# Optimization experiments

Measured on AMD Instinct MI355X. Metric: run time of the kernel, lower is better.

## Reference

```python
import jax, jax.numpy as jnp
import numpy as np

NEG_SLOPE = 0.2


def setup_inputs() -> dict:
    key = jax.random.key(0)
    k1, k2, k3 = jax.random.split(key, 3)
    bs, n_agents, input_dim = 32, 512, 128
    n_heads, hidden_dim = 8, 64
    h = jax.random.normal(k1, (bs, n_agents, input_dim), dtype=jnp.float32)
    # Linear(input_dim, n_heads*hidden_dim, bias=False), stored as [in, out]
    W = jax.random.normal(k2, (input_dim, n_heads * hidden_dim), dtype=jnp.float32) * (1.0 / np.sqrt(input_dim))
    # xavier_uniform with gain=1.414 on shape (1, n_heads, 2*hidden_dim)
    fan = n_heads + 2 * hidden_dim
    bound = 1.414 * np.sqrt(6.0 / fan)
    att_a = jax.random.uniform(k3, (1, n_heads, 2 * hidden_dim), dtype=jnp.float32,
                               minval=-bound, maxval=bound)
    return {"h": h, "W": W, "att_a": att_a}


def reference(h, W, att_a):
    bs, n_agents, _ = h.shape
    n_heads = att_a.shape[1]
    hidden_dim = att_a.shape[2] // 2
    # h_prime: [bs, n_heads, n_agents, hidden_dim]
    h_prime = (h @ W).reshape(bs, n_agents, n_heads, hidden_dim).transpose(0, 2, 1, 3)
    # Additive score decomposes exactly: (a1.h_i + a2.h_j) == sum(cat(h_i,h_j)*a)
    a_src = att_a[0, :, :hidden_dim]   # [n_heads, hidden_dim]
    a_dst = att_a[0, :, hidden_dim:]   # [n_heads, hidden_dim]
    e_src = jnp.einsum('bhnd,hd->bhn', h_prime, a_src)  # score contribution of node i (row)
    e_dst = jnp.einsum('bhnd,hd->bhn', h_prime, a_dst)  # contribution of node j (col)
    e = e_src[:, :, :, None] + e_dst[:, :, None, :]     # [bs, n_heads, n, n]
    e = jnp.where(e >= 0, e, NEG_SLOPE * e)             # leaky_relu(0.2)
    attention = jax.nn.softmax(e, axis=-1)
    h_new = jnp.einsum('bhnm,bhmd->bhnd', attention, h_prime)
    return jax.nn.elu(h_new)
```

## Files before the change

### kernel.cpp

```cpp
#include <hip/hip_runtime.h>

#define BS 32
#define NA 512
#define ID 128
#define NH 8
#define HD 64
#define NHD 512
#define NEG 0.2f
#define NC 32
#define CH 16

__global__ __launch_bounds__(256) void k1_gemm(
    const float* __restrict__ h, const float* __restrict__ W,
    const float* __restrict__ att, float* __restrict__ hp,
    float* __restrict__ s_out, float* __restrict__ t_out) {
  int blk = blockIdx.x;
  int b = blk >> 5;
  int n0 = (blk & 31) * 16;
  int t = threadIdx.x;
  int lane = t & 63, w = t >> 6;
  int r0 = __builtin_amdgcn_readfirstlane((w >> 1) * 8);
  int chalf = __builtin_amdgcn_readfirstlane(w & 1);
  int col = chalf * 256 + lane * 4;
  int head = col >> 6;
  int d0 = col & 63;
  const float* arow = h + ((size_t)b * NA + n0 + r0) * ID;
  const float* wptr = W + col;

  float4 a0c = {0,0,0,0}, a1c = {0,0,0,0}, a2c = {0,0,0,0}, a3c = {0,0,0,0};
  float4 a4c = {0,0,0,0}, a5c = {0,0,0,0}, a6c = {0,0,0,0}, a7c = {0,0,0,0};

#define K1_ROW(I, C, KK)                                                      \
  { float a_ = arow[(I) * ID + kc + (KK)];                                    \
    C.x += a_ * wv.x; C.y += a_ * wv.y; C.z += a_ * wv.z; C.w += a_ * wv.w; }
  #pragma unroll 1
  for (int kc = 0; kc < ID; kc += 8) {
    #pragma unroll
    for (int kk = 0; kk < 8; ++kk) {
      float4 wv = *(const float4*)(wptr + (size_t)(kc + kk) * NHD);
      K1_ROW(0, a0c, kk) K1_ROW(1, a1c, kk) K1_ROW(2, a2c, kk)
      K1_ROW(3, a3c, kk) K1_ROW(4, a4c, kk) K1_ROW(5, a5c, kk)
      K1_ROW(6, a6c, kk) K1_ROW(7, a7c, kk)
    }
  }
#undef K1_ROW
  {
    size_t off = ((((size_t)b * NH + head) * NA) + (n0 + r0)) * HD + d0;
    *(float4*)(hp + off) = a0c; off += HD;
    *(float4*)(hp + off) = a1c; off += HD;
    *(float4*)(hp + off) = a2c; off += HD;
    *(float4*)(hp + off) = a3c; off += HD;
    *(float4*)(hp + off) = a4c; off += HD;
    *(float4*)(hp + off) = a5c; off += HD;
    *(float4*)(hp + off) = a6c; off += HD;
    *(float4*)(hp + off) = a7c;
  }
  {
    float4 as4 = *(const float4*)(att + head * 128 + d0);
    float4 ad4 = *(const float4*)(att + head * 128 + 64 + d0);
#define DOT4(C, A) ((C).x*(A).x + (C).y*(A).y + (C).z*(A).z + (C).w*(A).w)
    float sp0 = DOT4(a0c, as4), tp0 = DOT4(a0c, ad4);
    float sp1 = DOT4(a1c, as4), tp1 = DOT4(a1c, ad4);
    float sp2 = DOT4(a2c, as4), tp2 = DOT4(a2c, ad4);
    float sp3 = DOT4(a3c, as4), tp3 = DOT4(a3c, ad4);
    float sp4 = DOT4(a4c, as4), tp4 = DOT4(a4c, ad4);
    float sp5 = DOT4(a5c, as4), tp5 = DOT4(a5c, ad4);
    float sp6 = DOT4(a6c, as4), tp6 = DOT4(a6c, ad4);
    float sp7 = DOT4(a7c, as4), tp7 = DOT4(a7c, ad4);
#undef DOT4
    #pragma unroll
    for (int m = 1; m < 16; m <<= 1) {
      sp0 += __shfl_xor(sp0, m, 64); tp0 += __shfl_xor(tp0, m, 64);
      sp1 += __shfl_xor(sp1, m, 64); tp1 += __shfl_xor(tp1, m, 64);
      sp2 += __shfl_xor(sp2, m, 64); tp2 += __shfl_xor(tp2, m, 64);
      sp3 += __shfl_xor(sp3, m, 64); tp3 += __shfl_xor(tp3, m, 64);
      sp4 += __shfl_xor(sp4, m, 64); tp4 += __shfl_xor(tp4, m, 64);
      sp5 += __shfl_xor(sp5, m, 64); tp5 += __shfl_xor(tp5, m, 64);
      sp6 += __shfl_xor(sp6, m, 64); tp6 += __shfl_xor(tp6, m, 64);
      sp7 += __shfl_xor(sp7, m, 64); tp7 += __shfl_xor(tp7, m, 64);
    }
    int g16 = lane & 15;
    int rsel = g16 & 7;
    float sv_ = rsel == 0 ? sp0 : rsel == 1 ? sp1 : rsel == 2 ? sp2 :
                rsel == 3 ? sp3 : rsel == 4 ? sp4 : rsel == 5 ? sp5 :
                rsel == 6 ? sp6 : sp7;
    float tv_ = rsel == 0 ? tp0 : rsel == 1 ? tp1 : rsel == 2 ? tp2 :
                rsel == 3 ? tp3 : rsel == 4 ? tp4 : rsel == 5 ? tp5 :
                rsel == 6 ? tp6 : tp7;
    size_t off = (((size_t)b * NH + head) * NA) + n0 + r0 + rsel;
    if (g16 < 8) s_out[off] = sv_;
    else         t_out[off] = tv_;
  }
}

__global__ __launch_bounds__(512) void k2_fused(
    const float* __restrict__ hp, const float* __restrict__ s_g,
    const float* __restrict__ t_g, float* __restrict__ out) {
  __shared__ float tv[NA]; __shared__ int tpm[NA];
  __shared__ float sv[NA]; __shared__ int spm[NA];
  __shared__ float wp[NA]; __shared__ float wn[NA];
  __shared__ float localP[8 * 64]; __shared__ float localN[8 * 64];
  __shared__ float seedP[8 * 64];  __shared__ float seedN[8 * 64];
  __shared__ float totP[64];
  __shared__ float zps[NA + 1]; __shared__ float znp[NA + 1];
  __shared__ float szP[NC]; __shared__ float szN[NC];
  __shared__ float sufZ[NC + 1]; __shared__ float preZ[NC + 1];
  __shared__ float aA[NA]; __shared__ float aB[NA]; __shared__ float aI[NA];
  __shared__ int aJ[NA]; __shared__ int aR[NA];

  int bh = blockIdx.x;
  int t = threadIdx.x;
  int lane = t & 63, w = t >> 6;
  const float* vbase = hp + (size_t)bh * NA * HD;

  float tvr = t_g[(size_t)bh * NA + t]; int tir = t;
  float svr = s_g[(size_t)bh * NA + t]; int sir = t;
  for (int size = 2; size <= NA; size <<= 1) {
    bool dirAsc = ((t & size) == 0);
    for (int stride = size >> 1; stride > 0; stride >>= 1) {
      float ptv, psv; int pti, psi;
      if (stride >= 64) {
        tv[t] = tvr; tpm[t] = tir; sv[t] = svr; spm[t] = sir;
        __syncthreads();
        ptv = tv[t ^ stride]; pti = tpm[t ^ stride];
        psv = sv[t ^ stride]; psi = spm[t ^ stride];
        __syncthreads();
      } else {
        ptv = __shfl_xor(tvr, stride, 64); pti = __shfl_xor(tir, stride, 64);
        psv = __shfl_xor(svr, stride, 64); psi = __shfl_xor(sir, stride, 64);
      }
      bool mn = (((t & stride) == 0) == dirAsc);
      bool swt = mn ? (ptv < tvr) : (ptv > tvr);
      if (swt) { tvr = ptv; tir = pti; }
      bool sws = mn ? (psv > svr) : (psv < svr);
      if (sws) { svr = psv; sir = psi; }
    }
  }
  tv[t] = tvr; tpm[t] = tir; sv[t] = svr; spm[t] = sir;
  __syncthreads();

  float cmax = fmaxf(tv[NA - 1], 0.f);
  float amax = fmaxf(sv[0], 0.f);
  wp[t] = __expf(tv[t] - cmax);
  wn[t] = __expf(NEG * tv[t] - cmax);
  __syncthreads();

  if (t < 32) {
    float a = 0.f;
    for (int j = t * CH; j < t * CH + CH; ++j) a += wp[j];
    szP[t] = a;
  } else if (t < 64) {
    int c = t - 32; float a = 0.f;
    for (int j = c * CH; j < c * CH + CH; ++j) a += wn[j];
    szN[c] = a;
  }
  {
    float aP = 0.f, aN = 0.f;
    int jb = w * 64;
    for (int jj = 0; jj < 64; ++jj) {
      int j = jb + jj;
      float vv = vbase[(size_t)tpm[j] * HD + lane];
      aP += wp[j] * vv;
      aN += wn[j] * vv;
    }
    localP[w * 64 + lane] = aP;
    localN[w * 64 + lane] = aN;
  }
  __syncthreads();

  if (t == 0) {
    float run = 0.f; sufZ[NC] = 0.f;
    for (int cc = NC - 1; cc >= 0; --cc) { run += szP[cc]; sufZ[cc] = run; }
  } else if (t == 1) {
    float run = 0.f;
    for (int cc = 0; cc <= NC; ++cc) { preZ[cc] = run; if (cc < NC) run += szN[cc]; }
  } else if (t >= 64 && t < 128) {
    int d = t - 64;
    float run = 0.f;
    for (int u = 0; u < 8; ++u) { seedP[u * 64 + d] = run; run += localP[u * 64 + d]; }
    totP[d] = run;
    float run2 = 0.f;
    for (int u = 0; u < 8; ++u) { seedN[u * 64 + d] = run2; run2 += localN[u * 64 + d]; }
  }
  __syncthreads();

  {
    int ch = t >> 4;
    float a = 0.f;
    for (int k = t; k < ch * CH + CH; ++k) a += wp[k];
    zps[t] = a + sufZ[ch + 1];
    float b2 = 0.f;
    for (int k = ch * CH; k < t; ++k) b2 += wn[k];
    znp[t] = preZ[ch] + b2;
    if (t == 0) { zps[NA] = 0.f; znp[NA] = preZ[NC]; }
  }
  __syncthreads();

  {
    float sval = sv[t];
    float A = __expf(sval - amax);
    float B = __expf(NEG * sval - amax);
    float key = -sval;
    int lo = 0, hi = NA;
    while (lo < hi) { int mid = (lo + hi) >> 1; if (tv[mid] < key) lo = mid + 1; else hi = mid; }
    float den = A * zps[lo] + B * znp[lo];
    aA[t] = A; aB[t] = B; aI[t] = 1.f / den; aJ[t] = lo; aR[t] = spm[t];
  }
  __syncthreads();

  {
    int jlo = w * 64, jhi = jlo + 64;
    int p;
    { int lo = 0, hi = NA;
      while (lo < hi) { int mid = (lo + hi) >> 1; if (aJ[mid] < jlo) lo = mid + 1; else hi = mid; }
      p = lo; }
    float prePr = seedP[w * 64 + lane];
    float preNr = seedN[w * 64 + lane];
    float totPd = totP[lane];
    for (int j = jlo; j < jhi; ++j) {
      while (p < NA && aJ[p] == j) {
        float A = aA[p], B = aB[p], inv = aI[p]; int row = aR[p];
        float x = (A * (totPd - prePr) + B * preNr) * inv;
        out[((size_t)bh * NA + row) * HD + lane] = x > 0.f ? x : __expf(x) - 1.f;
        ++p;
      }
      float vv = vbase[(size_t)tpm[j] * HD + lane];
      prePr += wp[j] * vv;
      preNr += wn[j] * vv;
    }
    if (w == 7) {
      while (p < NA) {
        float A = aA[p], B = aB[p], inv = aI[p]; int row = aR[p];
        float x = (A * (totPd - prePr) + B * preNr) * inv;
        out[((size_t)bh * NA + row) * HD + lane] = x > 0.f ? x : __expf(x) - 1.f;
        ++p;
      }
    }
  }
}

extern "C" void kernel_launch(void* const* d_in, const int* in_sizes, int n_in,
                              void* d_out, int out_size, void* d_ws, size_t ws_size,
                              hipStream_t stream) {
  const float* h  = (const float*)d_in[0];
  const float* W  = (const float*)d_in[1];
  const float* att = (const float*)d_in[2];
  float* out = (float*)d_out;
  float* hp    = (float*)d_ws;
  float* s_arr = hp + (size_t)BS * NH * NA * HD;
  float* t_arr = s_arr + (size_t)BS * NH * NA;

  k1_gemm <<<dim3(1024), dim3(256), 0, stream>>>(h, W, att, hp, s_arr, t_arr);
  k2_fused<<<dim3(256),  dim3(512), 0, stream>>>(hp, s_arr, t_arr, out);
}
```

Measured before the change: 157.4 us.

## Split fused attention kernel into sort, segment-local sums, and emit kernels

The single fused per-(batch,head) kernel is split into three launches. The first sorts and writes per-row metadata to global memory, the second computes per-segment weighted partial sums, and the third seeds prefix sums and emits outputs. Work is cut into 16 segments of 32 instead of 8 of 64, and k2b/k2c run 1024 blocks instead of 256, which raises parallelism and occupancy on the serial scan-and-emit phase. The cost is two extra launches and extra global round-trips for the index, weight and row-info arrays.

```diff
diff --git a/kernel.cpp b/kernel.cpp
--- a/kernel.cpp
+++ b/kernel.cpp
@@ -9,6 +9,8 @@
 #define NEG 0.2f
 #define NC 32
 #define CH 16
+#define NSEG 16
+#define SEG 32
 
 __global__ __launch_bounds__(256) void k1_gemm(
     const float* __restrict__ h, const float* __restrict__ W,
@@ -93,25 +95,20 @@
   }
 }
 
-__global__ __launch_bounds__(512) void k2_fused(
-    const float* __restrict__ hp, const float* __restrict__ s_g,
-    const float* __restrict__ t_g, float* __restrict__ out) {
+__global__ __launch_bounds__(512) void k2a_sort(
+    const float* __restrict__ s_g, const float* __restrict__ t_g,
+    int* __restrict__ tpm_g, float* __restrict__ wp_g, float* __restrict__ wn_g,
+    float4* __restrict__ rinfo_g, int* __restrict__ segStart_g) {
   __shared__ float tv[NA]; __shared__ int tpm[NA];
   __shared__ float sv[NA]; __shared__ int spm[NA];
   __shared__ float wp[NA]; __shared__ float wn[NA];
-  __shared__ float localP[8 * 64]; __shared__ float localN[8 * 64];
-  __shared__ float seedP[8 * 64];  __shared__ float seedN[8 * 64];
-  __shared__ float totP[64];
+  __shared__ int aJ[NA];
   __shared__ float zps[NA + 1]; __shared__ float znp[NA + 1];
   __shared__ float szP[NC]; __shared__ float szN[NC];
   __shared__ float sufZ[NC + 1]; __shared__ float preZ[NC + 1];
-  __shared__ float aA[NA]; __shared__ float aB[NA]; __shared__ float aI[NA];
-  __shared__ int aJ[NA]; __shared__ int aR[NA];
 
   int bh = blockIdx.x;
   int t = threadIdx.x;
-  int lane = t & 63, w = t >> 6;
-  const float* vbase = hp + (size_t)bh * NA * HD;
 
   float tvr = t_g[(size_t)bh * NA + t]; int tir = t;
   float svr = s_g[(size_t)bh * NA + t]; int sir = t;
@@ -141,8 +138,12 @@
 
   float cmax = fmaxf(tv[NA - 1], 0.f);
   float amax = fmaxf(sv[0], 0.f);
-  wp[t] = __expf(tv[t] - cmax);
-  wn[t] = __expf(NEG * tv[t] - cmax);
+  float wpv = __expf(tv[t] - cmax);
+  float wnv = __expf(NEG * tv[t] - cmax);
+  wp[t] = wpv; wn[t] = wnv;
+  tpm_g[(size_t)bh * NA + t] = tpm[t];
+  wp_g[(size_t)bh * NA + t] = wpv;
+  wn_g[(size_t)bh * NA + t] = wnv;
   __syncthreads();
 
   if (t < 32) {
@@ -154,36 +155,15 @@
     for (int j = c * CH; j < c * CH + CH; ++j) a += wn[j];
     szN[c] = a;
   }
-  {
-    float aP = 0.f, aN = 0.f;
-    int jb = w * 64;
-    for (int jj = 0; jj < 64; ++jj) {
-      int j = jb + jj;
-      float vv = vbase[(size_t)tpm[j] * HD + lane];
-      aP += wp[j] * vv;
-      aN += wn[j] * vv;
-    }
-    localP[w * 64 + lane] = aP;
-    localN[w * 64 + lane] = aN;
-  }
-  __syncthreads();
-
+  __syncthreads();
   if (t == 0) {
     float run = 0.f; sufZ[NC] = 0.f;
     for (int cc = NC - 1; cc >= 0; --cc) { run += szP[cc]; sufZ[cc] = run; }
   } else if (t == 1) {
     float run = 0.f;
     for (int cc = 0; cc <= NC; ++cc) { preZ[cc] = run; if (cc < NC) run += szN[cc]; }
-  } else if (t >= 64 && t < 128) {
-    int d = t - 64;
-    float run = 0.f;
-    for (int u = 0; u < 8; ++u) { seedP[u * 64 + d] = run; run += localP[u * 64 + d]; }
-    totP[d] = run;
-    float run2 = 0.f;
-    for (int u = 0; u < 8; ++u) { seedN[u * 64 + d] = run2; run2 += localN[u * 64 + d]; }
-  }
-  __syncthreads();
-
+  }
+  __syncthreads();
   {
     int ch = t >> 4;
     float a = 0.f;
@@ -198,43 +178,120 @@
 
   {
     float sval = sv[t];
+    int row = spm[t];
     float A = __expf(sval - amax);
     float B = __expf(NEG * sval - amax);
     float key = -sval;
     int lo = 0, hi = NA;
     while (lo < hi) { int mid = (lo + hi) >> 1; if (tv[mid] < key) lo = mid + 1; else hi = mid; }
     float den = A * zps[lo] + B * znp[lo];
-    aA[t] = A; aB[t] = B; aI[t] = 1.f / den; aJ[t] = lo; aR[t] = spm[t];
-  }
-  __syncthreads();
-
-  {
-    int jlo = w * 64, jhi = jlo + 64;
-    int p;
-    { int lo = 0, hi = NA;
-      while (lo < hi) { int mid = (lo + hi) >> 1; if (aJ[mid] < jlo) lo = mid + 1; else hi = mid; }
-      p = lo; }
-    float prePr = seedP[w * 64 + lane];
-    float preNr = seedN[w * 64 + lane];
-    float totPd = totP[lane];
-    for (int j = jlo; j < jhi; ++j) {
-      while (p < NA && aJ[p] == j) {
-        float A = aA[p], B = aB[p], inv = aI[p]; int row = aR[p];
-        float x = (A * (totPd - prePr) + B * preNr) * inv;
-        out[((size_t)bh * NA + row) * HD + lane] = x > 0.f ? x : __expf(x) - 1.f;
-        ++p;
-      }
-      float vv = vbase[(size_t)tpm[j] * HD + lane];
-      prePr += wp[j] * vv;
-      preNr += wn[j] * vv;
-    }
-    if (w == 7) {
-      while (p < NA) {
-        float A = aA[p], B = aB[p], inv = aI[p]; int row = aR[p];
-        float x = (A * (totPd - prePr) + B * preNr) * inv;
-        out[((size_t)bh * NA + row) * HD + lane] = x > 0.f ? x : __expf(x) - 1.f;
-        ++p;
-      }
+    float4 ri;
+    ri.x = A; ri.y = B; ri.z = 1.f / den;
+    ri.w = __int_as_float(lo | (row << 16));
+    rinfo_g[(size_t)bh * NA + t] = ri;
+    aJ[t] = lo;
+  }
+  __syncthreads();
+
+  if (t <= NSEG) {
+    int target = t * SEG;
+    int lo = 0, hi = NA;
+    while (lo < hi) { int mid = (lo + hi) >> 1; if (aJ[mid] < target) lo = mid + 1; else hi = mid; }
+    segStart_g[bh * (NSEG + 1) + t] = lo;
+  }
+}
+
+__global__ __launch_bounds__(256) void k2b_local(
+    const float* __restrict__ hp, const int* __restrict__ tpm_g,
+    const float* __restrict__ wp_g, const float* __restrict__ wn_g,
+    float* __restrict__ localP_g, float* __restrict__ localN_g) {
+  int blk = blockIdx.x;
+  int bh = blk >> 2;
+  int t = threadIdx.x;
+  int lane = t & 63, w = t >> 6;
+  int seg = (blk & 3) * 4 + w;
+  int jb = seg * SEG;
+  const float* vb = hp + (size_t)bh * NA * HD;
+  const int* tpb = tpm_g + (size_t)bh * NA;
+  const float* wpb = wp_g + (size_t)bh * NA;
+  const float* wnb = wn_g + (size_t)bh * NA;
+  float aP0 = 0.f, aP1 = 0.f, aP2 = 0.f, aP3 = 0.f;
+  float aN0 = 0.f, aN1 = 0.f, aN2 = 0.f, aN3 = 0.f;
+  #pragma unroll
+  for (int i = 0; i < SEG; i += 4) {
+    int j = jb + i;
+    int4 tp4 = *(const int4*)(tpb + j);
+    float4 wp4 = *(const float4*)(wpb + j);
+    float4 wn4 = *(const float4*)(wnb + j);
+    float v0 = vb[(size_t)tp4.x * HD + lane];
+    float v1 = vb[(size_t)tp4.y * HD + lane];
+    float v2 = vb[(size_t)tp4.z * HD + lane];
+    float v3 = vb[(size_t)tp4.w * HD + lane];
+    aP0 += wp4.x * v0; aN0 += wn4.x * v0;
+    aP1 += wp4.y * v1; aN1 += wn4.y * v1;
+    aP2 += wp4.z * v2; aN2 += wn4.z * v2;
+    aP3 += wp4.w * v3; aN3 += wn4.w * v3;
+  }
+  localP_g[((size_t)bh * NSEG + seg) * 64 + lane] = (aP0 + aP1) + (aP2 + aP3);
+  localN_g[((size_t)bh * NSEG + seg) * 64 + lane] = (aN0 + aN1) + (aN2 + aN3);
+}
+
+__global__ __launch_bounds__(256) void k2c_emit(
+    const float* __restrict__ hp, const int* __restrict__ tpm_g,
+    const float* __restrict__ wp_g, const float* __restrict__ wn_g,
+    const float* __restrict__ localP_g, const float* __restrict__ localN_g,
+    const float4* __restrict__ rinfo_g, const int* __restrict__ segStart_g,
+    float* __restrict__ out) {
+  int blk = blockIdx.x;
+  int bh = blk >> 2;
+  int t = threadIdx.x;
+  int lane = t & 63, w = t >> 6;
+  int seg = (blk & 3) * 4 + w;
+  int jb = seg * SEG;
+  const float* vb = hp + (size_t)bh * NA * HD;
+  const int* tpb = tpm_g + (size_t)bh * NA;
+  const float* wpb = wp_g + (size_t)bh * NA;
+  const float* wnb = wn_g + (size_t)bh * NA;
+  const float4* rib = rinfo_g + (size_t)bh * NA;
+  float* ob = out + (size_t)bh * NA * HD;
+
+  const float* lp = localP_g + (size_t)bh * NSEG * 64 + lane;
+  const float* ln = localN_g + (size_t)bh * NSEG * 64 + lane;
+  float seedP = 0.f, seedN = 0.f, totP = 0.f;
+  #pragma unroll
+  for (int u = 0; u < NSEG; ++u) {
+    float xp = lp[u * 64];
+    totP += xp;
+    if (u < seg) { seedP += xp; seedN += ln[u * 64]; }
+  }
+
+  int p  = segStart_g[bh * (NSEG + 1) + seg];
+  int p1 = segStart_g[bh * (NSEG + 1) + seg + 1];
+  float runP = seedP, runN = seedN;
+  for (int jj = 0; jj < SEG; ++jj) {
+    int j = jb + jj;
+    while (p < p1) {
+      float4 ri = rib[p];
+      int bits = __float_as_int(ri.w);
+      if ((bits & 0xFFFF) != j) break;
+      int row = bits >> 16;
+      float x = (ri.x * (totP - runP) + ri.y * runN) * ri.z;
+      ob[(size_t)row * HD + lane] = x > 0.f ? x : __expf(x) - 1.f;
+      ++p;
+    }
+    int vr = tpb[j];
+    float v = vb[(size_t)vr * HD + lane];
+    runP += wpb[j] * v;
+    runN += wnb[j] * v;
+  }
+  if (seg == NSEG - 1) {
+    while (p < NA) {
+      float4 ri = rib[p];
+      int bits = __float_as_int(ri.w);
+      int row = bits >> 16;
+      float x = (ri.x * (totP - runP) + ri.y * runN) * ri.z;
+      ob[(size_t)row * HD + lane] = x > 0.f ? x : __expf(x) - 1.f;
+      ++p;
     }
   }
 }
@@ -249,7 +306,20 @@
   float* hp    = (float*)d_ws;
   float* s_arr = hp + (size_t)BS * NH * NA * HD;
   float* t_arr = s_arr + (size_t)BS * NH * NA;
+  int*   tpm_g = (int*)(t_arr + (size_t)BS * NH * NA);
+  float* wp_g  = (float*)(tpm_g + (size_t)BS * NH * NA);
+  float* wn_g  = wp_g + (size_t)BS * NH * NA;
+  float* rinfo = wn_g + (size_t)BS * NH * NA;
+  int*   segS  = (int*)(rinfo + (size_t)BS * NH * NA * 4);
+  float* locP  = (float*)(segS + (size_t)BS * NH * 32);
+  float* locN  = locP + (size_t)BS * NH * NSEG * 64;
 
   k1_gemm <<<dim3(1024), dim3(256), 0, stream>>>(h, W, att, hp, s_arr, t_arr);
-  k2_fused<<<dim3(256),  dim3(512), 0, stream>>>(hp, s_arr, t_arr, out);
-}
+  k2a_sort<<<dim3(256),  dim3(512), 0, stream>>>(s_arr, t_arr, tpm_g, wp_g,
+                                                 wn_g, (float4*)rinfo, segS);
+  k2b_local<<<dim3(1024), dim3(256), 0, stream>>>(hp, tpm_g, wp_g, wn_g,
+                                                  locP, locN);
+  k2c_emit <<<dim3(1024), dim3(256), 0, stream>>>(hp, tpm_g, wp_g, wn_g,
+                                                  locP, locN, (float4*)rinfo,
+                                                  segS, out);
+}
```

Result: slower. 183.0 us (+16.2%).
